# Kernel tuning notes

Hardware: AMD Instinct MI355X
Metric: run time of the kernel (lower is better)

Reference implementation:

```python
import jax, jax.numpy as jnp
import numpy as np

N, E = 50000, 800000
D_IN, D_H, D_OUT = 128, 128, 64


def _gcn_conv(h, src, dst, norm, b, n):
    # h already linearly transformed: aggregate norm-weighted messages to dst
    msg = h[src] * norm[:, None]                      # [E+N, d]
    out = jax.ops.segment_sum(msg, dst, num_segments=n)
    return out + b


def setup_inputs() -> dict:
    key = jax.random.key(0)
    ks = jax.random.split(key, 5)
    x = jax.random.normal(ks[0], (N, D_IN), jnp.float32)
    edge_index = jax.random.randint(ks[1], (2, E), 0, N, jnp.int32)
    s1 = 1.0 / np.sqrt(D_IN)
    s2 = 1.0 / np.sqrt(D_H)
    W1 = jax.random.uniform(ks[2], (D_IN, D_H), jnp.float32, -s1, s1)
    b1 = jnp.zeros((D_H,), jnp.float32)
    W2 = jax.random.uniform(ks[3], (D_H, D_OUT), jnp.float32, -s2, s2)
    b2 = jnp.zeros((D_OUT,), jnp.float32)
    return {"x": x, "edge_index": edge_index, "W1": W1, "b1": b1, "W2": W2, "b2": b2}


def reference(x, edge_index, W1, b1, W2, b2):
    n = x.shape[0]
    loops = jnp.arange(n, dtype=edge_index.dtype)
    src = jnp.concatenate([edge_index[0], loops])     # add self-loops
    dst = jnp.concatenate([edge_index[1], loops])
    # symmetric normalization D^{-1/2} (A+I) D^{-1/2}; deg is in-degree incl. self-loop
    deg = jax.ops.segment_sum(jnp.ones(dst.shape[0], x.dtype), dst, num_segments=n)
    dinv = jnp.where(deg > 0, jax.lax.rsqrt(deg), 0.0)
    norm = dinv[src] * dinv[dst]
    h = _gcn_conv(x @ W1, src, dst, norm, b1, n)
    h = jax.nn.relu(h)                                # dropout = identity (eval)
    out = _gcn_conv(h @ W2, src, dst, norm, b2, n)
    return out
```

## Files before the change

kernel.cpp:

```cpp
#include <hip/hip_runtime.h>

typedef __bf16 bf16x8 __attribute__((ext_vector_type(8)));
typedef float  f32x4  __attribute__((ext_vector_type(4)));
typedef unsigned long long u64;

constexpr int PAD       = 64;
constexpr int BIN_SHIFT = 9;
constexpr int CAP       = 12288;
constexpr int SUBS      = 4;
constexpr int NPS       = 128;
constexpr int STR       = 68;
constexpr int CUR_STR   = 16;


__global__ void init_k(int* __restrict__ bincur, __bf16* __restrict__ h1zero,
                       __bf16* __restrict__ h3zero) {
  int t = threadIdx.x;
  for (int i = t; i < 128 * CUR_STR; i += 256) bincur[i] = 0;
  if (t < 128) h1zero[t] = (__bf16)0.f;
  if (t < 64)  h3zero[t] = (__bf16)0.f;
}


__global__ __launch_bounds__(256) void fused_bin_gemm_k(
    const int* __restrict__ src, const int* __restrict__ dst,
    int* __restrict__ bincur, u64* __restrict__ bin_data, int E,
    const float* __restrict__ X, const float* __restrict__ W,
    __bf16* __restrict__ C, int n) {
  constexpr int K   = 128;
  constexpr int KP  = K + 8;
  constexpr int NC  = 128;
  constexpr int NT  = NC / 16;
  constexpr int KC  = K / 32;

  __shared__ __align__(16) char smem[NC * KP * 2];

  const int t = threadIdx.x;

  {
    u64* pairs = (u64*)smem;
    int* binof = (int*)(smem + 8192);
    int* hist  = (int*)(smem + 12288);
    int* cur   = (int*)(smem + 12800);
    int* sbase = (int*)(smem + 13312);
    int* gbase = (int*)(smem + 13824);
    const int NB = (n + ((1 << BIN_SHIFT) - 1)) >> BIN_SHIFT;

    if (t < 128) { hist[t] = 0; cur[t] = 0; }
    __syncthreads();

    int base_e = (blockIdx.x * 256 + t) * 4;
    int m = E - base_e;
    m = m < 0 ? 0 : (m > 4 ? 4 : m);

    int sa[4], da[4], ba[4];
    if (m == 4) {
      int4 s4 = *reinterpret_cast<const int4*>(src + base_e);
      int4 d4 = *reinterpret_cast<const int4*>(dst + base_e);
      sa[0] = s4.x; sa[1] = s4.y; sa[2] = s4.z; sa[3] = s4.w;
      da[0] = d4.x; da[1] = d4.y; da[2] = d4.z; da[3] = d4.w;
    } else {
      for (int k = 0; k < m; ++k) { sa[k] = src[base_e + k]; da[k] = dst[base_e + k]; }
    }
    for (int k = 0; k < m; ++k) {
      ba[k] = da[k] >> BIN_SHIFT;
      atomicAdd(&hist[ba[k]], 1);
    }
    __syncthreads();

    if (t < 128) sbase[t] = hist[t];
    __syncthreads();
    for (int off = 1; off < 128; off <<= 1) {
      int u = (t >= off && t < 128) ? sbase[t - off] : 0;
      __syncthreads();
      if (t < 128) sbase[t] += u;
      __syncthreads();
    }
    if (t < NB && hist[t] > 0) gbase[t] = atomicAdd(&bincur[t * CUR_STR], hist[t]);
    if (t < 128) sbase[t] -= hist[t];
    __syncthreads();

    for (int k = 0; k < m; ++k) {
      int b = ba[k];
      int q = atomicAdd(&cur[b], 1);
      int slot = sbase[b] + q;
      pairs[slot] = ((u64)(unsigned)sa[k] << 32) | (unsigned)da[k];
      binof[slot] = b;
    }
    __syncthreads();

    int T = E - blockIdx.x * 1024;
    T = T > 1024 ? 1024 : T;
    for (int i = t; i < T; i += 256) {
      int b = binof[i];
      int pos = gbase[b] + (i - sbase[b]);
      if (pos < CAP) bin_data[(size_t)b * CAP + pos] = pairs[i];
    }
    __syncthreads();
  }

  __bf16* WT = (__bf16*)smem;
  for (int idx = t; idx < K * (NC / 4); idx += 256) {
    int k  = idx / (NC / 4);
    int c4 = idx % (NC / 4);
    f32x4 v = reinterpret_cast<const f32x4*>(W)[idx];
    WT[(c4 * 4 + 0) * KP + k] = (__bf16)v[0];
    WT[(c4 * 4 + 1) * KP + k] = (__bf16)v[1];
    WT[(c4 * 4 + 2) * KP + k] = (__bf16)v[2];
    WT[(c4 * 4 + 3) * KP + k] = (__bf16)v[3];
  }
  __syncthreads();

  const int lane = t & 63;
  const int lr = lane & 15;
  const int lg = lane >> 4;

  const int mt = blockIdx.x * 4 + (t >> 6);
  const int mtiles = (n + 15) / 16;
  if (mt >= mtiles) return;

  bf16x8 bfrag[NT][KC];
#pragma unroll
  for (int nt = 0; nt < NT; ++nt)
#pragma unroll
    for (int kc = 0; kc < KC; ++kc)
      bfrag[nt][kc] = *reinterpret_cast<const bf16x8*>(
          &WT[(nt * 16 + lr) * KP + kc * 32 + lg * 8]);

  const int row  = mt * 16 + lr;
  const int crow = (row < n) ? row : (n - 1);

  bf16x8 afrag[KC];
#pragma unroll
  for (int kc = 0; kc < KC; ++kc) {
    const f32x4* p = reinterpret_cast<const f32x4*>(
        X + (size_t)crow * K + kc * 32 + lg * 8);
    f32x4 v0 = p[0], v1 = p[1];
    bf16x8 a;
    a[0] = (__bf16)v0[0]; a[1] = (__bf16)v0[1];
    a[2] = (__bf16)v0[2]; a[3] = (__bf16)v0[3];
    a[4] = (__bf16)v1[0]; a[5] = (__bf16)v1[1];
    a[6] = (__bf16)v1[2]; a[7] = (__bf16)v1[3];
    afrag[kc] = a;
  }

  f32x4 acc[NT];
#pragma unroll
  for (int nt = 0; nt < NT; ++nt) acc[nt] = (f32x4){0.f, 0.f, 0.f, 0.f};
#pragma unroll
  for (int kc = 0; kc < KC; ++kc)
#pragma unroll
    for (int nt = 0; nt < NT; ++nt)
      acc[nt] = __builtin_amdgcn_mfma_f32_16x16x32_bf16(afrag[kc], bfrag[nt][kc],
                                                        acc[nt], 0, 0, 0);

#pragma unroll
  for (int nt = 0; nt < NT; ++nt)
#pragma unroll
    for (int r = 0; r < 4; ++r) {
      int orow = mt * 16 + lg * 4 + r;
      if (orow < n) C[(size_t)orow * NC + nt * 16 + lr] = (__bf16)acc[nt][r];
    }
}


__global__ __launch_bounds__(512) void csr_build_k(const int* __restrict__ bincur,
                                                   const u64* __restrict__ bin_data,
                                                   int* __restrict__ srcs_pad,
                                                   int* __restrict__ cnt,
                                                   float* __restrict__ dinv,
                                                   __bf16* __restrict__ h1b, int n) {
  __shared__ int rows[NPS * STR];
  __shared__ int lcnt[NPS];

  const int bin = blockIdx.x / SUBS;
  const int sub = blockIdx.x % SUBS;
  const int lo  = (bin << BIN_SHIFT) + sub * NPS;
  const int hi  = min(n, (bin + 1) << BIN_SHIFT);

  for (int i = threadIdx.x; i < NPS * STR; i += 512) rows[i] = n;
  for (int i = threadIdx.x; i < NPS; i += 512) lcnt[i] = 0;
  __syncthreads();

  int cntE = bincur[bin * CUR_STR];
  cntE = cntE < CAP ? cntE : CAP;
  const u64* bd = bin_data + (size_t)bin * CAP;

  for (int i = threadIdx.x; i < cntE; i += 512) {
    u64 p = bd[i];
    int d = (int)(p & 0xffffffffu);
    unsigned l = (unsigned)(d - lo);
    if (l < (unsigned)NPS) {
      int q = atomicAdd(&lcnt[l], 1);
      if (q < PAD) rows[l * STR + q] = (int)(p >> 32);
    }
  }
  __syncthreads();

  for (int i = threadIdx.x; i < NPS * (PAD / 4); i += 512) {
    int nl = i >> 4;
    int c4 = i & 15;
    int g = lo + nl;
    if (g < hi)
      *reinterpret_cast<int4*>(&srcs_pad[(size_t)g * PAD + c4 * 4]) =
          *reinterpret_cast<const int4*>(&rows[nl * STR + c4 * 4]);
  }
  for (int i = threadIdx.x; i < NPS; i += 512) {
    int g = lo + i;
    if (g < hi) {
      int c = lcnt[i];
      cnt[g] = c;
      dinv[g] = rsqrtf((float)(c + 1));
    }
  }
  bf16x8* h8 = reinterpret_cast<bf16x8*>(h1b);
  for (int i = threadIdx.x; i < NPS * 16; i += 512) {
    int nl = i >> 4;
    int c8 = i & 15;
    int g = lo + nl;
    if (g < hi) {
      float di = rsqrtf((float)(lcnt[nl] + 1));
      bf16x8 v = h8[(size_t)g * 16 + c8];
      bf16x8 o;
#pragma unroll
      for (int q = 0; q < 8; ++q) o[q] = (__bf16)((float)v[q] * di);
      h8[(size_t)g * 16 + c8] = o;
    }
  }
}


__global__ __launch_bounds__(256) void gather_gemm2_k(
    const __bf16* __restrict__ h1b, const int* __restrict__ cnt,
    const int* __restrict__ srcs_pad, const float* __restrict__ dinv,
    const float* __restrict__ b1, const float* __restrict__ W2,
    __bf16* __restrict__ h3b, int n) {
  constexpr int K  = 128;
  constexpr int KP = K + 8;
  constexpr int NT = 4;
  constexpr int KC = 4;

  __shared__ __bf16 W2T[64 * KP];
  __shared__ __bf16 aggT[64 * KP];

  const int t = threadIdx.x;

  for (int idx = t; idx < K * 16; idx += 256) {
    int k  = idx / 16;
    int c4 = idx % 16;
    f32x4 v = reinterpret_cast<const f32x4*>(W2)[idx];
    W2T[(c4 * 4 + 0) * KP + k] = (__bf16)v[0];
    W2T[(c4 * 4 + 1) * KP + k] = (__bf16)v[1];
    W2T[(c4 * 4 + 2) * KP + k] = (__bf16)v[2];
    W2T[(c4 * 4 + 3) * KP + k] = (__bf16)v[3];
  }

  const int base = blockIdx.x * 64;
  const bf16x8* h8 = reinterpret_cast<const bf16x8*>(h1b);
#pragma unroll
  for (int pass = 0; pass < 4; ++pass) {
    const int nl = pass * 16 + (t >> 4);
    const int d8 = t & 15;
    const int node = base + nl;
    bf16x8 ov;
    if (node < n) {
      int c = cnt[node];
      c = c < PAD ? c : PAD;
      const float di = dinv[node];
      const int* row = srcs_pad + (size_t)node * PAD;
      bf16x8 sv = h8[(size_t)node * 16 + d8];

      float acc[8];
#pragma unroll
      for (int q = 0; q < 8; ++q) acc[q] = 0.f;

      for (int j0 = 0; j0 < c; j0 += 8) {
        int4 a = *reinterpret_cast<const int4*>(row + j0);
        int4 b = *reinterpret_cast<const int4*>(row + j0 + 4);
        bf16x8 v0 = h8[(size_t)a.x * 16 + d8];
        bf16x8 v1 = h8[(size_t)a.y * 16 + d8];
        bf16x8 v2 = h8[(size_t)a.z * 16 + d8];
        bf16x8 v3 = h8[(size_t)a.w * 16 + d8];
        bf16x8 v4 = h8[(size_t)b.x * 16 + d8];
        bf16x8 v5 = h8[(size_t)b.y * 16 + d8];
        bf16x8 v6 = h8[(size_t)b.z * 16 + d8];
        bf16x8 v7 = h8[(size_t)b.w * 16 + d8];
#pragma unroll
        for (int q = 0; q < 8; ++q)
          acc[q] += ((float)v0[q] + (float)v1[q]) + ((float)v2[q] + (float)v3[q]) +
                    ((float)v4[q] + (float)v5[q]) + ((float)v6[q] + (float)v7[q]);
      }
#pragma unroll
      for (int q = 0; q < 8; ++q) {
        float val = (acc[q] + (float)sv[q]) * di + b1[d8 * 8 + q];
        ov[q] = (__bf16)fmaxf(val, 0.f);
      }
    } else {
#pragma unroll
      for (int q = 0; q < 8; ++q) ov[q] = (__bf16)0.f;
    }
    *reinterpret_cast<bf16x8*>(&aggT[nl * KP + d8 * 8]) = ov;
  }
  __syncthreads();

  const int lane = t & 63;
  const int lr = lane & 15;
  const int lg = lane >> 4;
  const int wv = t >> 6;

  bf16x8 bfrag[NT][KC];
#pragma unroll
  for (int nt = 0; nt < NT; ++nt)
#pragma unroll
    for (int kc = 0; kc < KC; ++kc)
      bfrag[nt][kc] = *reinterpret_cast<const bf16x8*>(
          &W2T[(nt * 16 + lr) * KP + kc * 32 + lg * 8]);

  bf16x8 afrag[KC];
#pragma unroll
  for (int kc = 0; kc < KC; ++kc)
    afrag[kc] = *reinterpret_cast<const bf16x8*>(
        &aggT[(wv * 16 + lr) * KP + kc * 32 + lg * 8]);

  f32x4 acc[NT];
#pragma unroll
  for (int nt = 0; nt < NT; ++nt) acc[nt] = (f32x4){0.f, 0.f, 0.f, 0.f};
#pragma unroll
  for (int kc = 0; kc < KC; ++kc)
#pragma unroll
    for (int nt = 0; nt < NT; ++nt)
      acc[nt] = __builtin_amdgcn_mfma_f32_16x16x32_bf16(afrag[kc], bfrag[nt][kc],
                                                        acc[nt], 0, 0, 0);

#pragma unroll
  for (int r = 0; r < 4; ++r) {
    int orow = base + wv * 16 + lg * 4 + r;
    if (orow < n) {
      float sc = dinv[orow];
#pragma unroll
      for (int nt = 0; nt < NT; ++nt)
        h3b[(size_t)orow * 64 + nt * 16 + lr] = (__bf16)(acc[nt][r] * sc);
    }
  }
}


template<int D, bool RELU_OUT, bool OUT_BF16>
__global__ __launch_bounds__(256) void gather_bf_k(const __bf16* __restrict__ h,
                                                   const int* __restrict__ cnt,
                                                   const int* __restrict__ srcs_pad,
                                                   const float* __restrict__ dinv,
                                                   const float* __restrict__ bias,
                                                   void* __restrict__ outv, int n) {
  constexpr int L = D / 8;
  int t = blockIdx.x * 256 + threadIdx.x;
  int node = t / L;
  int d8 = t % L;
  if (node >= n) return;

  int c = cnt[node];
  c = c < PAD ? c : PAD;
  const float di = dinv[node];
  const int* row = srcs_pad + (size_t)node * PAD;
  const bf16x8* h8 = reinterpret_cast<const bf16x8*>(h);
  bf16x8 sv = h8[(size_t)node * L + d8];

  float acc[8];
#pragma unroll
  for (int q = 0; q < 8; ++q) acc[q] = 0.f;

  for (int j0 = 0; j0 < c; j0 += 8) {
    int4 a = *reinterpret_cast<const int4*>(row + j0);
    int4 b = *reinterpret_cast<const int4*>(row + j0 + 4);
    bf16x8 v0 = h8[(size_t)a.x * L + d8];
    bf16x8 v1 = h8[(size_t)a.y * L + d8];
    bf16x8 v2 = h8[(size_t)a.z * L + d8];
    bf16x8 v3 = h8[(size_t)a.w * L + d8];
    bf16x8 v4 = h8[(size_t)b.x * L + d8];
    bf16x8 v5 = h8[(size_t)b.y * L + d8];
    bf16x8 v6 = h8[(size_t)b.z * L + d8];
    bf16x8 v7 = h8[(size_t)b.w * L + d8];
#pragma unroll
    for (int q = 0; q < 8; ++q)
      acc[q] += ((float)v0[q] + (float)v1[q]) + ((float)v2[q] + (float)v3[q]) +
                ((float)v4[q] + (float)v5[q]) + ((float)v6[q] + (float)v7[q]);
  }

  float o[8];
#pragma unroll
  for (int q = 0; q < 8; ++q) {
    float b = bias[d8 * 8 + q];
    float val = (acc[q] + (float)sv[q]) * di + b;
    o[q] = RELU_OUT ? fmaxf(val, 0.f) : val;
  }

  if (OUT_BF16) {
    bf16x8 ov;
#pragma unroll
    for (int q = 0; q < 8; ++q) ov[q] = (__bf16)o[q];
    reinterpret_cast<bf16x8*>(outv)[(size_t)node * L + d8] = ov;
  } else {
    f32x4 lo = {o[0], o[1], o[2], o[3]};
    f32x4 hi = {o[4], o[5], o[6], o[7]};
    f32x4* op = reinterpret_cast<f32x4*>((float*)outv + (size_t)node * D + d8 * 8);
    op[0] = lo;
    op[1] = hi;
  }
}


extern "C" void kernel_launch(void* const* d_in, const int* in_sizes, int n_in,
                              void* d_out, int out_size, void* d_ws, size_t ws_size,
                              hipStream_t stream) {
  const float* x  = (const float*)d_in[0];
  const int*   ei = (const int*)d_in[1];
  const float* W1 = (const float*)d_in[2];
  const float* b1 = (const float*)d_in[3];
  const float* W2 = (const float*)d_in[4];
  const float* b2 = (const float*)d_in[5];

  const int n = in_sizes[0] / 128;
  const int E = in_sizes[1] / 2;
  const int* src = ei;
  const int* dst = ei + E;
  float* out = (float*)d_out;

  const int NB = (n + ((1 << BIN_SHIFT) - 1)) >> BIN_SHIFT;

  int*   bincur   = (int*)d_ws;
  int*   cnt      = (int*)d_ws + 128 * CUR_STR;
  float* dinv     = (float*)d_ws + 128 * CUR_STR + n;
  int*   srcs_pad = (int*)d_ws + 128 * CUR_STR + 2 * n;
  size_t w = (size_t)128 * CUR_STR + 2 * n + (size_t)n * PAD;
  __bf16* h1b   = (__bf16*)((int*)d_ws + w);   w += (size_t)(n + 1) * 64;
  __bf16* scratch = (__bf16*)((int*)d_ws + w); w += (size_t)n * 64;
  __bf16* h3b   = (__bf16*)((int*)d_ws + w);
  u64* bin_data = (u64*)scratch;

  init_k<<<1, 256, 0, stream>>>(bincur, h1b + (size_t)n * 128, h3b + (size_t)n * 64);

  const int fillB = (E / 4 + 255) / 256;
  fused_bin_gemm_k<<<fillB, 256, 0, stream>>>(
      src, dst, bincur, bin_data, E, x, W1, h1b, n);

  csr_build_k<<<NB * SUBS, 512, 0, stream>>>(bincur, bin_data, srcs_pad, cnt, dinv, h1b, n);

  gather_gemm2_k<<<(n + 63) / 64, 256, 0, stream>>>(
      h1b, cnt, srcs_pad, dinv, b1, W2, h3b, n);

  {
    long long t = (long long)n * 8;
    gather_bf_k<64, false, false><<<(int)((t + 255) / 256), 256, 0, stream>>>(
        h3b, cnt, srcs_pad, dinv, b2, out, n);
  }
}
```

Before: 111.5 us.

## Split binning and GEMM1 into separate kernels with persistent GEMM grid

Splits the fused edge-binning and first GEMM kernel into two launches. Binning now handles 2048 edges per block instead of 1024, so fewer blocks share the global bin counters. GEMM1 runs on a persistent 256-block grid that loads W1 into shared memory once per block and loops over row tiles, so far fewer blocks repeat the transposed weight staging. The W transpose loads are rewritten to read columns and write 4 packed bf16 values at a time. The cost is an extra kernel launch and the loss of any overlap between binning and GEMM work that came from fusing them.

```diff
diff --git a/kernel.cpp b/kernel.cpp
--- a/kernel.cpp
+++ b/kernel.cpp
@@ -1,6 +1,7 @@
 #include <hip/hip_runtime.h>
 
 typedef __bf16 bf16x8 __attribute__((ext_vector_type(8)));
+typedef __bf16 bf16x4 __attribute__((ext_vector_type(4)));
 typedef float  f32x4  __attribute__((ext_vector_type(4)));
 typedef unsigned long long u64;
 
@@ -11,6 +12,7 @@
 constexpr int NPS       = 128;
 constexpr int STR       = 68;
 constexpr int CUR_STR   = 16;
+constexpr int EPB       = 2048;
 
 
 __global__ void init_k(int* __restrict__ bincur, __bf16* __restrict__ h1zero,
@@ -22,92 +24,89 @@
 }
 
 
-__global__ __launch_bounds__(256) void fused_bin_gemm_k(
+__global__ __launch_bounds__(256) void bin_fill_k(
     const int* __restrict__ src, const int* __restrict__ dst,
-    int* __restrict__ bincur, u64* __restrict__ bin_data, int E,
-    const float* __restrict__ X, const float* __restrict__ W,
-    __bf16* __restrict__ C, int n) {
-  constexpr int K   = 128;
-  constexpr int KP  = K + 8;
-  constexpr int NC  = 128;
-  constexpr int NT  = NC / 16;
-  constexpr int KC  = K / 32;
-
-  __shared__ __align__(16) char smem[NC * KP * 2];
+    int* __restrict__ bincur, u64* __restrict__ bin_data, int E, int n) {
+  __shared__ u64 pairs[EPB];
+  __shared__ int binof[EPB];
+  __shared__ int hist[128], cur[128], sbase[128], gbase[128];
 
   const int t = threadIdx.x;
-
-  {
-    u64* pairs = (u64*)smem;
-    int* binof = (int*)(smem + 8192);
-    int* hist  = (int*)(smem + 12288);
-    int* cur   = (int*)(smem + 12800);
-    int* sbase = (int*)(smem + 13312);
-    int* gbase = (int*)(smem + 13824);
-    const int NB = (n + ((1 << BIN_SHIFT) - 1)) >> BIN_SHIFT;
-
-    if (t < 128) { hist[t] = 0; cur[t] = 0; }
+  const int NB = (n + ((1 << BIN_SHIFT) - 1)) >> BIN_SHIFT;
+
+  if (t < 128) { hist[t] = 0; cur[t] = 0; }
+  __syncthreads();
+
+  int base_e = blockIdx.x * EPB + t * 8;
+  int m = E - base_e;
+  m = m < 0 ? 0 : (m > 8 ? 8 : m);
+
+  int sa[8], da[8], ba[8];
+  if (m == 8) {
+    int4 s0 = *reinterpret_cast<const int4*>(src + base_e);
+    int4 s1 = *reinterpret_cast<const int4*>(src + base_e + 4);
+    int4 d0 = *reinterpret_cast<const int4*>(dst + base_e);
+    int4 d1 = *reinterpret_cast<const int4*>(dst + base_e + 4);
+    sa[0]=s0.x; sa[1]=s0.y; sa[2]=s0.z; sa[3]=s0.w;
+    sa[4]=s1.x; sa[5]=s1.y; sa[6]=s1.z; sa[7]=s1.w;
+    da[0]=d0.x; da[1]=d0.y; da[2]=d0.z; da[3]=d0.w;
+    da[4]=d1.x; da[5]=d1.y; da[6]=d1.z; da[7]=d1.w;
+  } else {
+    for (int k = 0; k < m; ++k) { sa[k] = src[base_e + k]; da[k] = dst[base_e + k]; }
+  }
+  for (int k = 0; k < m; ++k) {
+    ba[k] = da[k] >> BIN_SHIFT;
+    atomicAdd(&hist[ba[k]], 1);
+  }
+  __syncthreads();
+
+  if (t < 128) sbase[t] = hist[t];
+  __syncthreads();
+  for (int off = 1; off < 128; off <<= 1) {
+    int u = (t >= off && t < 128) ? sbase[t - off] : 0;
     __syncthreads();
-
-    int base_e = (blockIdx.x * 256 + t) * 4;
-    int m = E - base_e;
-    m = m < 0 ? 0 : (m > 4 ? 4 : m);
-
-    int sa[4], da[4], ba[4];
-    if (m == 4) {
-      int4 s4 = *reinterpret_cast<const int4*>(src + base_e);
-      int4 d4 = *reinterpret_cast<const int4*>(dst + base_e);
-      sa[0] = s4.x; sa[1] = s4.y; sa[2] = s4.z; sa[3] = s4.w;
-      da[0] = d4.x; da[1] = d4.y; da[2] = d4.z; da[3] = d4.w;
-    } else {
-      for (int k = 0; k < m; ++k) { sa[k] = src[base_e + k]; da[k] = dst[base_e + k]; }
-    }
-    for (int k = 0; k < m; ++k) {
-      ba[k] = da[k] >> BIN_SHIFT;
-      atomicAdd(&hist[ba[k]], 1);
-    }
+    if (t < 128) sbase[t] += u;
     __syncthreads();
-
-    if (t < 128) sbase[t] = hist[t];
-    __syncthreads();
-    for (int off = 1; off < 128; off <<= 1) {
-      int u = (t >= off && t < 128) ? sbase[t - off] : 0;
-      __syncthreads();
-      if (t < 128) sbase[t] += u;
-      __syncthreads();
-    }
-    if (t < NB && hist[t] > 0) gbase[t] = atomicAdd(&bincur[t * CUR_STR], hist[t]);
-    if (t < 128) sbase[t] -= hist[t];
-    __syncthreads();
-
-    for (int k = 0; k < m; ++k) {
-      int b = ba[k];
-      int q = atomicAdd(&cur[b], 1);
-      int slot = sbase[b] + q;
-      pairs[slot] = ((u64)(unsigned)sa[k] << 32) | (unsigned)da[k];
-      binof[slot] = b;
-    }
-    __syncthreads();
-
-    int T = E - blockIdx.x * 1024;
-    T = T > 1024 ? 1024 : T;
-    for (int i = t; i < T; i += 256) {
-      int b = binof[i];
-      int pos = gbase[b] + (i - sbase[b]);
-      if (pos < CAP) bin_data[(size_t)b * CAP + pos] = pairs[i];
-    }
-    __syncthreads();
-  }
-
-  __bf16* WT = (__bf16*)smem;
-  for (int idx = t; idx < K * (NC / 4); idx += 256) {
-    int k  = idx / (NC / 4);
-    int c4 = idx % (NC / 4);
-    f32x4 v = reinterpret_cast<const f32x4*>(W)[idx];
-    WT[(c4 * 4 + 0) * KP + k] = (__bf16)v[0];
-    WT[(c4 * 4 + 1) * KP + k] = (__bf16)v[1];
-    WT[(c4 * 4 + 2) * KP + k] = (__bf16)v[2];
-    WT[(c4 * 4 + 3) * KP + k] = (__bf16)v[3];
+  }
+  if (t < NB && hist[t] > 0) gbase[t] = atomicAdd(&bincur[t * CUR_STR], hist[t]);
+  if (t < 128) sbase[t] -= hist[t];
+  __syncthreads();
+
+  for (int k = 0; k < m; ++k) {
+    int b = ba[k];
+    int q = atomicAdd(&cur[b], 1);
+    int slot = sbase[b] + q;
+    pairs[slot] = ((u64)(unsigned)sa[k] << 32) | (unsigned)da[k];
+    binof[slot] = b;
+  }
+  __syncthreads();
+
+  int T = E - blockIdx.x * EPB;
+  T = T > EPB ? EPB : T;
+  for (int i = t; i < T; i += 256) {
+    int b = binof[i];
+    int pos = gbase[b] + (i - sbase[b]);
+    if (pos < CAP) bin_data[(size_t)b * CAP + pos] = pairs[i];
+  }
+}
+
+
+__global__ __launch_bounds__(256) void gemm1_k(const float* __restrict__ X,
+                                               const float* __restrict__ W,
+                                               __bf16* __restrict__ C, int n) {
+  constexpr int K = 128, KP = 136, NC = 128, NT = 8, KC = 4;
+  __shared__ __bf16 WT[NC * KP];
+
+  const int t = threadIdx.x;
+  for (int idx = t; idx < K * NC / 4; idx += 256) {
+    int col = idx & 127;
+    int k4  = idx >> 7;
+    bf16x4 w;
+    w[0] = (__bf16)W[(k4 * 4 + 0) * NC + col];
+    w[1] = (__bf16)W[(k4 * 4 + 1) * NC + col];
+    w[2] = (__bf16)W[(k4 * 4 + 2) * NC + col];
+    w[3] = (__bf16)W[(k4 * 4 + 3) * NC + col];
+    *reinterpret_cast<bf16x4*>(&WT[col * KP + k4 * 4]) = w;
   }
   __syncthreads();
 
@@ -115,10 +114,6 @@
   const int lr = lane & 15;
   const int lg = lane >> 4;
 
-  const int mt = blockIdx.x * 4 + (t >> 6);
-  const int mtiles = (n + 15) / 16;
-  if (mt >= mtiles) return;
-
   bf16x8 bfrag[NT][KC];
 #pragma unroll
   for (int nt = 0; nt < NT; ++nt)
@@ -127,40 +122,46 @@
       bfrag[nt][kc] = *reinterpret_cast<const bf16x8*>(
           &WT[(nt * 16 + lr) * KP + kc * 32 + lg * 8]);
 
-  const int row  = mt * 16 + lr;
-  const int crow = (row < n) ? row : (n - 1);
-
-  bf16x8 afrag[KC];
-#pragma unroll
-  for (int kc = 0; kc < KC; ++kc) {
-    const f32x4* p = reinterpret_cast<const f32x4*>(
-        X + (size_t)crow * K + kc * 32 + lg * 8);
-    f32x4 v0 = p[0], v1 = p[1];
-    bf16x8 a;
-    a[0] = (__bf16)v0[0]; a[1] = (__bf16)v0[1];
-    a[2] = (__bf16)v0[2]; a[3] = (__bf16)v0[3];
-    a[4] = (__bf16)v1[0]; a[5] = (__bf16)v1[1];
-    a[6] = (__bf16)v1[2]; a[7] = (__bf16)v1[3];
-    afrag[kc] = a;
-  }
-
-  f32x4 acc[NT];
-#pragma unroll
-  for (int nt = 0; nt < NT; ++nt) acc[nt] = (f32x4){0.f, 0.f, 0.f, 0.f};
-#pragma unroll
-  for (int kc = 0; kc < KC; ++kc)
+  const int gw = blockIdx.x * 4 + (t >> 6);
+  const int nw = gridDim.x * 4;
+  const int mtiles = (n + 15) / 16;
+
+  for (int mt = gw; mt < mtiles; mt += nw) {
+    const int row  = mt * 16 + lr;
+    const int crow = (row < n) ? row : (n - 1);
+
+    bf16x8 afrag[KC];
+#pragma unroll
+    for (int kc = 0; kc < KC; ++kc) {
+      const f32x4* p = reinterpret_cast<const f32x4*>(
+          X + (size_t)crow * K + kc * 32 + lg * 8);
+      f32x4 v0 = p[0], v1 = p[1];
+      bf16x8 a;
+      a[0] = (__bf16)v0[0]; a[1] = (__bf16)v0[1];
+      a[2] = (__bf16)v0[2]; a[3] = (__bf16)v0[3];
+      a[4] = (__bf16)v1[0]; a[5] = (__bf16)v1[1];
+      a[6] = (__bf16)v1[2]; a[7] = (__bf16)v1[3];
+      afrag[kc] = a;
+    }
+
+    f32x4 acc[NT];
+#pragma unroll
+    for (int nt = 0; nt < NT; ++nt) acc[nt] = (f32x4){0.f, 0.f, 0.f, 0.f};
+#pragma unroll
+    for (int kc = 0; kc < KC; ++kc)
+#pragma unroll
+      for (int nt = 0; nt < NT; ++nt)
+        acc[nt] = __builtin_amdgcn_mfma_f32_16x16x32_bf16(afrag[kc], bfrag[nt][kc],
+                                                          acc[nt], 0, 0, 0);
+
 #pragma unroll
     for (int nt = 0; nt < NT; ++nt)
-      acc[nt] = __builtin_amdgcn_mfma_f32_16x16x32_bf16(afrag[kc], bfrag[nt][kc],
-                                                        acc[nt], 0, 0, 0);
-
-#pragma unroll
-  for (int nt = 0; nt < NT; ++nt)
-#pragma unroll
-    for (int r = 0; r < 4; ++r) {
-      int orow = mt * 16 + lg * 4 + r;
-      if (orow < n) C[(size_t)orow * NC + nt * 16 + lr] = (__bf16)acc[nt][r];
-    }
+#pragma unroll
+      for (int r = 0; r < 4; ++r) {
+        int orow = mt * 16 + lg * 4 + r;
+        if (orow < n) C[(size_t)orow * NC + nt * 16 + lr] = (__bf16)acc[nt][r];
+      }
+  }
 }
 
 
@@ -236,7 +237,7 @@
     const float* __restrict__ b1, const float* __restrict__ W2,
     __bf16* __restrict__ h3b, int n) {
   constexpr int K  = 128;
-  constexpr int KP = K + 8;
+  constexpr int KP = 136;
   constexpr int NT = 4;
   constexpr int KC = 4;
 
@@ -245,14 +246,15 @@
 
   const int t = threadIdx.x;
 
-  for (int idx = t; idx < K * 16; idx += 256) {
-    int k  = idx / 16;
-    int c4 = idx % 16;
-    f32x4 v = reinterpret_cast<const f32x4*>(W2)[idx];
-    W2T[(c4 * 4 + 0) * KP + k] = (__bf16)v[0];
-    W2T[(c4 * 4 + 1) * KP + k] = (__bf16)v[1];
-    W2T[(c4 * 4 + 2) * KP + k] = (__bf16)v[2];
-    W2T[(c4 * 4 + 3) * KP + k] = (__bf16)v[3];
+  for (int idx = t; idx < K * 64 / 4; idx += 256) {
+    int col = idx & 63;
+    int k4  = idx >> 6;
+    bf16x4 w;
+    w[0] = (__bf16)W2[(k4 * 4 + 0) * 64 + col];
+    w[1] = (__bf16)W2[(k4 * 4 + 1) * 64 + col];
+    w[2] = (__bf16)W2[(k4 * 4 + 2) * 64 + col];
+    w[3] = (__bf16)W2[(k4 * 4 + 3) * 64 + col];
+    *reinterpret_cast<bf16x4*>(&W2T[col * KP + k4 * 4]) = w;
   }
 
   const int base = blockIdx.x * 64;
@@ -432,16 +434,17 @@
   float* dinv     = (float*)d_ws + 128 * CUR_STR + n;
   int*   srcs_pad = (int*)d_ws + 128 * CUR_STR + 2 * n;
   size_t w = (size_t)128 * CUR_STR + 2 * n + (size_t)n * PAD;
-  __bf16* h1b   = (__bf16*)((int*)d_ws + w);   w += (size_t)(n + 1) * 64;
-  __bf16* scratch = (__bf16*)((int*)d_ws + w); w += (size_t)n * 64;
-  __bf16* h3b   = (__bf16*)((int*)d_ws + w);
+  __bf16* h1b     = (__bf16*)((int*)d_ws + w);   w += (size_t)(n + 1) * 64;
+  __bf16* scratch = (__bf16*)((int*)d_ws + w);   w += (size_t)n * 64;
+  __bf16* h3b     = (__bf16*)((int*)d_ws + w);
   u64* bin_data = (u64*)scratch;
 
   init_k<<<1, 256, 0, stream>>>(bincur, h1b + (size_t)n * 128, h3b + (size_t)n * 64);
 
-  const int fillB = (E / 4 + 255) / 256;
-  fused_bin_gemm_k<<<fillB, 256, 0, stream>>>(
-      src, dst, bincur, bin_data, E, x, W1, h1b, n);
+  const int fillB = (E + EPB - 1) / EPB;
+  bin_fill_k<<<fillB, 256, 0, stream>>>(src, dst, bincur, bin_data, E, n);
+
+  gemm1_k<<<256, 256, 0, stream>>>(x, W1, h1b, n);
 
   csr_build_k<<<NB * SUBS, 512, 0, stream>>>(bincur, bin_data, srcs_pad, cnt, dinv, h1b, n);
 
```

After: 104.0 us. 6.8% less time.
